# Kernel optimization log

Hardware: AMD Instinct MI355X
Metric: run time of the kernel (lower is better)

Reference implementation:

```python
import math
import jax, jax.numpy as jnp
import numpy as np

B, L, D_MODEL = 2, 2048, 1024
N_HEAD, HEAD_DIM = 16, 64
ATT_SCALE = 1.0  # divisor is sqrt(head_dim ** attention_scale)


def setup_inputs() -> dict:
    key = jax.random.key(0)
    ks = jax.random.split(key, 6)
    HD = N_HEAD * HEAD_DIM
    # Xavier-uniform style init for projection weights (stored as [in, out])
    def xavier(k, fan_in, fan_out):
        lim = math.sqrt(6.0 / (fan_in + fan_out))
        return jax.random.uniform(k, (fan_in, fan_out), jnp.float32, -lim, lim)
    return {
        "x":  jax.random.normal(ks[0], (B, L, D_MODEL), jnp.float32),
        "Wq": xavier(ks[1], D_MODEL, HD), "bq": jnp.zeros((HD,), jnp.float32),
        "Wk": xavier(ks[2], D_MODEL, HD), "bk": jnp.zeros((HD,), jnp.float32),
        "Wv": xavier(ks[3], D_MODEL, HD), "bv": jnp.zeros((HD,), jnp.float32),
        "Wo": xavier(ks[4], HD, D_MODEL),
        "bo": jax.random.uniform(ks[5], (D_MODEL,), jnp.float32, -1.0 / math.sqrt(HD), 1.0 / math.sqrt(HD)),
    }


def reference(x, Wq, bq, Wk, bk, Wv, bv, Wo, bo):
    b, l, _ = x.shape
    # QKV projections -> [B, L, H, Dh]
    q = (x @ Wq + bq).reshape(b, l, N_HEAD, HEAD_DIM)
    k = (x @ Wk + bk).reshape(b, l, N_HEAD, HEAD_DIM)
    v = (x @ Wv + bv).reshape(b, l, N_HEAD, HEAD_DIM)
    scale = 1.0 / math.sqrt(HEAD_DIM ** ATT_SCALE)
    # Unnormalized (no softmax) attention: (Q K^T / sqrt(Dh)) V
    scores = jnp.einsum("blhd,bmhd->bhlm", q, k) * scale  # [B,H,L,L]
    attn = jnp.einsum("bhlm,bmhd->blhd", scores, v)        # [B,L,H,Dh]
    out = attn.reshape(b, l, N_HEAD * HEAD_DIM) @ Wo + bo  # dispatcher
    return out
```

## Files before the change

### kernel.cpp

```cpp
#include <hip/hip_runtime.h>
#include <stdint.h>

#define B_ 2
#define L_ 2048
#define DM 1024
#define NH 16
#define DH 64
#define M_ (B_*L_)
#define NQKV 3072

typedef short short8 __attribute__((ext_vector_type(8)));
typedef float f32x4 __attribute__((ext_vector_type(4)));

__device__ __forceinline__ unsigned short f2b(float f) {
    union { float f; unsigned int u; } v; v.f = f;
    unsigned int u = v.u;
    return (unsigned short)((u + 0x7fffu + ((u >> 16) & 1u)) >> 16);
}

__device__ __forceinline__ void gld_lds16(const void* g, void* l) {
    __builtin_amdgcn_global_load_lds(
        (const __attribute__((address_space(1))) void*)g,
        (__attribute__((address_space(3))) void*)l, 16, 0, 0);
}

__global__ __launch_bounds__(256)
void setup_kernel(const float* __restrict__ x,
                  const float* __restrict__ Wq, const float* __restrict__ Wk,
                  const float* __restrict__ Wv, const float* __restrict__ Wo,
                  const float* __restrict__ bq, const float* __restrict__ bk,
                  const float* __restrict__ bv,
                  unsigned short* __restrict__ xb, unsigned short* __restrict__ WqkvT,
                  unsigned short* __restrict__ WoT, float* __restrict__ biasq,
                  float* __restrict__ KtV)
{
    __shared__ float tile[32][33];
    const int bid = blockIdx.x;
    const int t = threadIdx.x;

    if (bid < 2048) {
        int i = (bid * 256 + t) * 8;
        float4 a0 = *(const float4*)(x + i);
        float4 a1 = *(const float4*)(x + i + 4);
        uint4 p;
        p.x = (unsigned)f2b(a0.x) | ((unsigned)f2b(a0.y) << 16);
        p.y = (unsigned)f2b(a0.z) | ((unsigned)f2b(a0.w) << 16);
        p.z = (unsigned)f2b(a1.x) | ((unsigned)f2b(a1.y) << 16);
        p.w = (unsigned)f2b(a1.z) | ((unsigned)f2b(a1.w) << 16);
        *(uint4*)(xb + i) = p;
    } else if (bid < 2048 + 4096) {
        int wb = bid - 2048;
        int wi = wb >> 10;
        int tid = wb & 1023;
        const float* W = (wi == 0) ? Wq : (wi == 1) ? Wk : (wi == 2) ? Wv : Wo;
        float s = (wi == 1) ? 0.125f : 1.0f;
        int n0 = (tid & 31) * 32, k0 = (tid >> 5) * 32;
        int r = t >> 3, c4 = (t & 7) << 2;
        float4 v = *(const float4*)(W + (size_t)(k0 + r) * DM + n0 + c4);
        tile[r][c4+0] = v.x; tile[r][c4+1] = v.y; tile[r][c4+2] = v.z; tile[r][c4+3] = v.w;
        __syncthreads();
        uint2 o;
        o.x = (unsigned)f2b(tile[c4+0][r]*s) | ((unsigned)f2b(tile[c4+1][r]*s) << 16);
        o.y = (unsigned)f2b(tile[c4+2][r]*s) | ((unsigned)f2b(tile[c4+3][r]*s) << 16);
        int f = n0 + r;
        size_t drow;
        unsigned short* dst;
        if (wi == 0)      { dst = WqkvT; drow = f; }
        else if (wi == 1) { dst = WqkvT; drow = 1024 + (f >> 6) * 128 + (f & 63); }
        else if (wi == 2) { dst = WqkvT; drow = 1024 + (f >> 6) * 128 + 64 + (f & 63); }
        else              { dst = WoT;   drow = f; }
        *(uint2*)(dst + drow * DM + k0 + c4) = o;
    } else if (bid < 2048 + 4096 + 12) {
        int n = (bid - 6144) * 256 + t;
        float v;
        if (n < 1024) v = bq[n];
        else {
            int kv = (n - 1024) >> 7, r = (n - 1024) & 127;
            v = (r < 64) ? 0.125f * bk[kv * 64 + r] : bv[kv * 64 + (r - 64)];
        }
        biasq[n] = v;
    } else {
        int i = ((bid - 6156) * 256 + t) * 4;
        float4 z; z.x = z.y = z.z = z.w = 0.f;
        *(float4*)(KtV + i) = z;
    }
}

__global__ __launch_bounds__(256)
void qkv_fused_kernel(const unsigned short* __restrict__ A,
                      const unsigned short* __restrict__ Bt,
                      const float* __restrict__ biasq,
                      unsigned short* __restrict__ Qb,
                      float* __restrict__ KtV)
{
    __shared__ __align__(16) char smem[34816];
    unsigned short* As = (unsigned short*)smem;
    unsigned short* Bs = (unsigned short*)(smem + 8192);

    const int bid = blockIdx.x;
    const int xcd = bid & 7, local = bid >> 3;
    const int mt = xcd * 4 + (local & 3);
    const int nt = local >> 2;
    const int m0 = mt * 128, n0 = nt * 128;

    const int t = threadIdx.x;
    const int w = t >> 6, lane = t & 63;
    const int quad = lane >> 4, l16 = lane & 15;
    const int wm = w >> 1, wn = w & 1;

    f32x4 acc[4][4];
    #pragma unroll
    for (int i = 0; i < 4; i++)
        #pragma unroll
        for (int j = 0; j < 4; j++)
            #pragma unroll
            for (int r = 0; r < 4; r++) acc[i][j][r] = 0.f;

    const int srow = t >> 2;
    const int schunk = t & 3;

    for (int kk = 0; kk < DM; kk += 32) {
        #pragma unroll
        for (int p = 0; p < 2; p++) {
            int row = p * 64 + srow;
            int g = schunk ^ ((row >> 1) & 3);
            gld_lds16(A  + (size_t)(m0 + row) * DM + kk + g * 8,
                      (char*)As + p * 4096 + w * 1024);
            gld_lds16(Bt + (size_t)(n0 + row) * DM + kk + g * 8,
                      (char*)Bs + p * 4096 + w * 1024);
        }
        __syncthreads();

        short8 afr[4], bfr[4];
        #pragma unroll
        for (int i = 0; i < 4; i++) {
            int am = wm * 64 + i * 16 + l16;
            afr[i] = *(const short8*)((const char*)As + am * 64 + ((quad ^ ((am >> 1) & 3)) << 4));
            int bn = wn * 64 + i * 16 + l16;
            bfr[i] = *(const short8*)((const char*)Bs + bn * 64 + ((quad ^ ((bn >> 1) & 3)) << 4));
        }
        #pragma unroll
        for (int i = 0; i < 4; i++)
            #pragma unroll
            for (int j = 0; j < 4; j++)
                acc[i][j] = __builtin_amdgcn_mfma_f32_16x16x32_bf16(afr[i], bfr[j], acc[i][j], 0, 0, 0);
        __syncthreads();
    }

    #pragma unroll
    for (int j = 0; j < 4; j++) {
        float bv = biasq[n0 + wn * 64 + j * 16 + l16];
        #pragma unroll
        for (int i = 0; i < 4; i++)
            #pragma unroll
            for (int r = 0; r < 4; r++) acc[i][j][r] += bv;
    }

    if (nt < 8) {
        #pragma unroll
        for (int j = 0; j < 4; j++) {
            int col = n0 + wn * 64 + j * 16 + l16;
            #pragma unroll
            for (int i = 0; i < 4; i++) {
                #pragma unroll
                for (int r = 0; r < 4; r++) {
                    int row = m0 + wm * 64 + i * 16 + quad * 4 + r;
                    Qb[(size_t)row * DM + col] = f2b(acc[i][j][r]);
                }
            }
        }
        return;
    }

    const int h  = nt - 8;
    const int bh = (m0 >> 11) * NH + h;
    unsigned short (*Xt)[136] = (unsigned short (*)[136])smem;

    #pragma unroll
    for (int j = 0; j < 4; j++) {
        int c = wn * 64 + j * 16 + l16;
        #pragma unroll
        for (int i = 0; i < 4; i++) {
            int l0 = wm * 64 + i * 16 + quad * 4;
            uint2 o;
            o.x = (unsigned)f2b(acc[i][j][0]) | ((unsigned)f2b(acc[i][j][1]) << 16);
            o.y = (unsigned)f2b(acc[i][j][2]) | ((unsigned)f2b(acc[i][j][3]) << 16);
            *(uint2*)&Xt[c][l0] = o;
        }
    }
    __syncthreads();

    f32x4 kacc[4];
    #pragma unroll
    for (int j = 0; j < 4; j++)
        #pragma unroll
        for (int r = 0; r < 4; r++) kacc[j][r] = 0.f;

    #pragma unroll
    for (int ks = 0; ks < 4; ks++) {
        short8 af = *(const short8*)&Xt[w * 16 + l16][ks * 32 + quad * 8];
        #pragma unroll
        for (int j = 0; j < 4; j++) {
            short8 bfr = *(const short8*)&Xt[64 + j * 16 + l16][ks * 32 + quad * 8];
            kacc[j] = __builtin_amdgcn_mfma_f32_16x16x32_bf16(af, bfr, kacc[j], 0, 0, 0);
        }
    }

    float* dst = KtV + (size_t)bh * 64 * 64;
    #pragma unroll
    for (int j = 0; j < 4; j++) {
        int col = j * 16 + l16;
        #pragma unroll
        for (int r = 0; r < 4; r++) {
            int row = w * 16 + quad * 4 + r;
            atomicAdd(dst + row * 64 + col, kacc[j][r]);
        }
    }
}

__global__ __launch_bounds__(256)
void zmat_kernel(const unsigned short* __restrict__ WoT, const float* __restrict__ KtV,
                 unsigned short* __restrict__ ZT)
{
    __shared__ __align__(16) unsigned short Asl[64][72];
    __shared__ __align__(16) unsigned short Bsl[64][72];

    const int bh = blockIdx.x, nt0 = blockIdx.y;
    const int b = bh >> 4, h = bh & 15;
    const int t = threadIdx.x;
    const int wave = t >> 6, lane = t & 63;
    const int quad = lane >> 4, l16 = lane & 15;
    const int n0 = nt0 * 64;
    const int row = t >> 2, c0 = (t & 3) << 4;

    const unsigned short* ap = WoT + (size_t)(n0 + row) * DM + h * DH + c0;
    *(uint4*)&Asl[row][c0]     = *(const uint4*)ap;
    *(uint4*)&Asl[row][c0 + 8] = *(const uint4*)(ap + 8);

    const float* kp = KtV + ((size_t)bh * 64 + row) * 64 + c0;
    #pragma unroll
    for (int j = 0; j < 16; j++) Bsl[row][c0 + j] = f2b(kp[j]);
    __syncthreads();

    f32x4 acc[4];
    #pragma unroll
    for (int i = 0; i < 4; i++)
        #pragma unroll
        for (int r = 0; r < 4; r++) acc[i][r] = 0.f;

    #pragma unroll
    for (int ks = 0; ks < 2; ks++) {
        short8 af = *(const short8*)&Asl[wave * 16 + l16][ks * 32 + quad * 8];
        #pragma unroll
        for (int nt = 0; nt < 4; nt++) {
            short8 bfr = *(const short8*)&Bsl[nt * 16 + l16][ks * 32 + quad * 8];
            acc[nt] = __builtin_amdgcn_mfma_f32_16x16x32_bf16(af, bfr, acc[nt], 0, 0, 0);
        }
    }

    unsigned short* zb = ZT + (size_t)b * 1024 * 1024 + (size_t)h * DH;
    #pragma unroll
    for (int nt = 0; nt < 4; nt++) {
        int col = nt * 16 + l16;
        #pragma unroll
        for (int r = 0; r < 4; r++) {
            int zr = n0 + wave * 16 + quad * 4 + r;
            zb[(size_t)zr * 1024 + col] = f2b(acc[nt][r]);
        }
    }
}

__global__ __launch_bounds__(256)
void out_gemm_kernel(const unsigned short* __restrict__ A,
                     const unsigned short* __restrict__ Bt,
                     const float* __restrict__ bias,
                     float* __restrict__ C)
{
    __shared__ __align__(16) unsigned short As[128 * 64];
    __shared__ __align__(16) unsigned short Bs[64 * 64];

    const int bid = blockIdx.x;
    const int xcd = bid & 7, local = bid >> 3;
    const int mt = xcd * 4 + (local & 3);
    const int nt = local >> 2;
    const int m0 = mt * 128, n0 = nt * 64;

    const int t = threadIdx.x;
    const int w = t >> 6, lane = t & 63;
    const int quad = lane >> 4, l16 = lane & 15;

    const unsigned short* Btb = Bt + (size_t)(m0 >> 11) * 1024 * 1024;

    f32x4 acc[2][4];
    #pragma unroll
    for (int i = 0; i < 2; i++)
        #pragma unroll
        for (int j = 0; j < 4; j++)
            #pragma unroll
            for (int r = 0; r < 4; r++) acc[i][j][r] = 0.f;

    for (int kk = 0; kk < DM; kk += 64) {
        #pragma unroll
        for (int p = 0; p < 4; p++) {
            int c = p * 256 + t;
            int row = c >> 3, slot = c & 7;
            int g = slot ^ ((row >> 1) & 7);
            gld_lds16(A + (size_t)(m0 + row) * DM + kk + g * 8,
                      (char*)As + p * 4096 + w * 1024);
        }
        #pragma unroll
        for (int p = 0; p < 2; p++) {
            int c = p * 256 + t;
            int row = c >> 3, slot = c & 7;
            int g = slot ^ ((row >> 1) & 7);
            gld_lds16(Btb + (size_t)(n0 + row) * DM + kk + g * 8,
                      (char*)Bs + p * 4096 + w * 1024);
        }
        __syncthreads();

        #pragma unroll
        for (int ks = 0; ks < 2; ks++) {
            int kc = ks * 4 + quad;
            short8 afr[2], bfr[4];
            #pragma unroll
            for (int i = 0; i < 2; i++) {
                int am = w * 32 + i * 16 + l16;
                afr[i] = *(const short8*)((const char*)As + am * 128 + ((kc ^ ((am >> 1) & 7)) << 4));
            }
            #pragma unroll
            for (int j = 0; j < 4; j++) {
                int bn = j * 16 + l16;
                bfr[j] = *(const short8*)((const char*)Bs + bn * 128 + ((kc ^ ((bn >> 1) & 7)) << 4));
            }
            #pragma unroll
            for (int i = 0; i < 2; i++)
                #pragma unroll
                for (int j = 0; j < 4; j++)
                    acc[i][j] = __builtin_amdgcn_mfma_f32_16x16x32_bf16(afr[i], bfr[j], acc[i][j], 0, 0, 0);
        }
        __syncthreads();
    }

    #pragma unroll
    for (int j = 0; j < 4; j++) {
        int col = n0 + j * 16 + l16;
        float bv = bias[col];
        #pragma unroll
        for (int i = 0; i < 2; i++) {
            #pragma unroll
            for (int r = 0; r < 4; r++) {
                int row = m0 + w * 32 + i * 16 + quad * 4 + r;
                C[(size_t)row * DM + col] = acc[i][j][r] + bv;
            }
        }
    }
}


extern "C" void kernel_launch(void* const* d_in, const int* in_sizes, int n_in,
                              void* d_out, int out_size, void* d_ws, size_t ws_size,
                              hipStream_t stream)
{
    const float* x  = (const float*)d_in[0];
    const float* Wq = (const float*)d_in[1];
    const float* bq = (const float*)d_in[2];
    const float* Wk = (const float*)d_in[3];
    const float* bk = (const float*)d_in[4];
    const float* Wv = (const float*)d_in[5];
    const float* bv = (const float*)d_in[6];
    const float* Wo = (const float*)d_in[7];
    const float* bo = (const float*)d_in[8];

    char* ws = (char*)d_ws;
    unsigned short* xb    = (unsigned short*)(ws);
    unsigned short* WqkvT = (unsigned short*)(ws + (size_t)8  * 1024 * 1024);
    unsigned short* WoT   = (unsigned short*)(ws + (size_t)14 * 1024 * 1024);
    float*          biasq = (float*)         (ws + (size_t)16 * 1024 * 1024);
    unsigned short* Qb    = (unsigned short*)(ws + (size_t)17 * 1024 * 1024);
    unsigned short* ZT    = (unsigned short*)(ws + (size_t)25 * 1024 * 1024);
    float*          KtV   = (float*)         (ws + (size_t)29 * 1024 * 1024);

    setup_kernel<<<6284, 256, 0, stream>>>(x, Wq, Wk, Wv, Wo, bq, bk, bv,
                                           xb, WqkvT, WoT, biasq, KtV);

    qkv_fused_kernel<<<768, 256, 0, stream>>>(xb, WqkvT, biasq, Qb, KtV);

    zmat_kernel<<<dim3(B_ * NH, 16), 256, 0, stream>>>(WoT, KtV, ZT);

    out_gemm_kernel<<<512, 256, 0, stream>>>(Qb, ZT, bo, (float*)d_out);
}
```

Baseline: 143.3 us.

## Enlarge QKV GEMM tiles to 256x256 with double-buffered async LDS prefetch

The fused QKV GEMM now uses 256x256 output tiles with 512 threads, a 64-wide K step and two LDS buffers. Global-to-LDS loads for the next K step are issued while the current step's MFMAs run, with explicit vmcnt waits and barriers. The transposed K/V epilogue is reworked for two heads per tile and uses XOR-swizzled LDS. The aim is more data reuse per block and hidden load latency. In exchange only 192 blocks launch, which may underfill the GPU's CUs, and the 128 KB of LDS with the large accumulator array limits occupancy.

Measured after the change: 148.1 us. +3.4%, slower.

```diff
diff --git a/kernel.cpp b/kernel.cpp
--- a/kernel.cpp
+++ b/kernel.cpp
@@ -86,85 +86,112 @@
     }
 }
 
-__global__ __launch_bounds__(256)
+__global__ __launch_bounds__(512, 2)
 void qkv_fused_kernel(const unsigned short* __restrict__ A,
                       const unsigned short* __restrict__ Bt,
                       const float* __restrict__ biasq,
                       unsigned short* __restrict__ Qb,
                       float* __restrict__ KtV)
 {
-    __shared__ __align__(16) char smem[34816];
-    unsigned short* As = (unsigned short*)smem;
-    unsigned short* Bs = (unsigned short*)(smem + 8192);
+    __shared__ __align__(16) char smem[131072];
 
     const int bid = blockIdx.x;
-    const int xcd = bid & 7, local = bid >> 3;
-    const int mt = xcd * 4 + (local & 3);
-    const int nt = local >> 2;
-    const int m0 = mt * 128, n0 = nt * 128;
+    const int mt = bid & 15;
+    const int nt = bid >> 4;
+    const int m0 = mt * 256, n0 = nt * 256;
 
     const int t = threadIdx.x;
     const int w = t >> 6, lane = t & 63;
     const int quad = lane >> 4, l16 = lane & 15;
-    const int wm = w >> 1, wn = w & 1;
-
-    f32x4 acc[4][4];
-    #pragma unroll
-    for (int i = 0; i < 4; i++)
+    const int wr = w >> 2, wc = w & 3;
+
+    f32x4 acc[8][4];
+    #pragma unroll
+    for (int i = 0; i < 8; i++)
         #pragma unroll
         for (int j = 0; j < 4; j++)
             #pragma unroll
             for (int r = 0; r < 4; r++) acc[i][j][r] = 0.f;
 
-    const int srow = t >> 2;
-    const int schunk = t & 3;
-
-    for (int kk = 0; kk < DM; kk += 32) {
-        #pragma unroll
-        for (int p = 0; p < 2; p++) {
-            int row = p * 64 + srow;
-            int g = schunk ^ ((row >> 1) & 3);
-            gld_lds16(A  + (size_t)(m0 + row) * DM + kk + g * 8,
-                      (char*)As + p * 4096 + w * 1024);
+    auto STAGE = [&](int buf, int kk) {
+        #pragma unroll
+        for (int p = 0; p < 4; p++) {
+            int c = p * 512 + t;
+            int row = c >> 3, slot = c & 7;
+            int g = slot ^ ((row >> 1) & 7);
+            gld_lds16(A + (size_t)(m0 + row) * DM + kk + g * 8,
+                      smem + buf * 65536 + p * 8192 + w * 1024);
+        }
+        #pragma unroll
+        for (int p = 0; p < 4; p++) {
+            int c = p * 512 + t;
+            int row = c >> 3, slot = c & 7;
+            int g = slot ^ ((row >> 1) & 7);
             gld_lds16(Bt + (size_t)(n0 + row) * DM + kk + g * 8,
-                      (char*)Bs + p * 4096 + w * 1024);
-        }
-        __syncthreads();
-
-        short8 afr[4], bfr[4];
-        #pragma unroll
-        for (int i = 0; i < 4; i++) {
-            int am = wm * 64 + i * 16 + l16;
-            afr[i] = *(const short8*)((const char*)As + am * 64 + ((quad ^ ((am >> 1) & 3)) << 4));
-            int bn = wn * 64 + i * 16 + l16;
-            bfr[i] = *(const short8*)((const char*)Bs + bn * 64 + ((quad ^ ((bn >> 1) & 3)) << 4));
-        }
-        #pragma unroll
-        for (int i = 0; i < 4; i++)
-            #pragma unroll
-            for (int j = 0; j < 4; j++)
-                acc[i][j] = __builtin_amdgcn_mfma_f32_16x16x32_bf16(afr[i], bfr[j], acc[i][j], 0, 0, 0);
-        __syncthreads();
+                      smem + buf * 65536 + 32768 + p * 8192 + w * 1024);
+        }
+    };
+
+    STAGE(0, 0);
+    STAGE(1, 64);
+    asm volatile("s_waitcnt vmcnt(8)" ::: "memory");
+    __builtin_amdgcn_sched_barrier(0);
+    __builtin_amdgcn_s_barrier();
+
+    for (int T = 0; T < 16; T++) {
+        const char* Ab = smem + (T & 1) * 65536;
+        const char* Bb = Ab + 32768;
+        #pragma unroll
+        for (int kf = 0; kf < 2; kf++) {
+            int kc = kf * 4 + quad;
+            short8 af[8], bf[4];
+            #pragma unroll
+            for (int i = 0; i < 8; i++) {
+                int am = wr * 128 + i * 16 + l16;
+                af[i] = *(const short8*)(Ab + am * 128 + ((kc ^ ((am >> 1) & 7)) << 4));
+            }
+            #pragma unroll
+            for (int j = 0; j < 4; j++) {
+                int bn = wc * 64 + j * 16 + l16;
+                bf[j] = *(const short8*)(Bb + bn * 128 + ((kc ^ ((bn >> 1) & 7)) << 4));
+            }
+            #pragma unroll
+            for (int i = 0; i < 8; i++)
+                #pragma unroll
+                for (int j = 0; j < 4; j++)
+                    acc[i][j] = __builtin_amdgcn_mfma_f32_16x16x32_bf16(af[i], bf[j], acc[i][j], 0, 0, 0);
+        }
+        __builtin_amdgcn_sched_barrier(0);
+        __builtin_amdgcn_s_barrier();
+        if (T < 14) {
+            STAGE(T & 1, (T + 2) * 64);
+            __builtin_amdgcn_sched_barrier(0);
+            asm volatile("s_waitcnt vmcnt(8)" ::: "memory");
+        } else {
+            asm volatile("s_waitcnt vmcnt(0)" ::: "memory");
+        }
+        __builtin_amdgcn_sched_barrier(0);
+        __builtin_amdgcn_s_barrier();
     }
 
     #pragma unroll
     for (int j = 0; j < 4; j++) {
-        float bv = biasq[n0 + wn * 64 + j * 16 + l16];
-        #pragma unroll
-        for (int i = 0; i < 4; i++)
+        float bv = biasq[n0 + wc * 64 + j * 16 + l16];
+        #pragma unroll
+        for (int i = 0; i < 8; i++)
             #pragma unroll
             for (int r = 0; r < 4; r++) acc[i][j][r] += bv;
     }
 
-    if (nt < 8) {
+    if (nt < 4) {
         #pragma unroll
         for (int j = 0; j < 4; j++) {
-            int col = n0 + wn * 64 + j * 16 + l16;
-            #pragma unroll
-            for (int i = 0; i < 4; i++) {
+            int col = n0 + wc * 64 + j * 16 + l16;
+            #pragma unroll
+            for (int i = 0; i < 8; i++) {
                 #pragma unroll
                 for (int r = 0; r < 4; r++) {
-                    int row = m0 + wm * 64 + i * 16 + quad * 4 + r;
+                    int row = m0 + wr * 128 + i * 16 + quad * 4 + r;
                     Qb[(size_t)row * DM + col] = f2b(acc[i][j][r]);
                 }
             }
@@ -172,23 +199,26 @@
         return;
     }
 
-    const int h  = nt - 8;
-    const int bh = (m0 >> 11) * NH + h;
-    unsigned short (*Xt)[136] = (unsigned short (*)[136])smem;
-
     #pragma unroll
     for (int j = 0; j < 4; j++) {
-        int c = wn * 64 + j * 16 + l16;
-        #pragma unroll
-        for (int i = 0; i < 4; i++) {
-            int l0 = wm * 64 + i * 16 + quad * 4;
+        int c = wc * 64 + j * 16 + l16;
+        int cs = (c & 7) << 4;
+        #pragma unroll
+        for (int i = 0; i < 8; i++) {
+            int l0 = wr * 128 + i * 16 + quad * 4;
             uint2 o;
             o.x = (unsigned)f2b(acc[i][j][0]) | ((unsigned)f2b(acc[i][j][1]) << 16);
             o.y = (unsigned)f2b(acc[i][j][2]) | ((unsigned)f2b(acc[i][j][3]) << 16);
-            *(uint2*)&Xt[c][l0] = o;
-        }
-    }
-    __syncthreads();
+            *(uint2*)(smem + c * 512 + ((l0 * 2) ^ cs)) = o;
+        }
+    }
+    __builtin_amdgcn_sched_barrier(0);
+    __builtin_amdgcn_s_barrier();
+
+    const int hh = w >> 2;
+    const int s  = w & 3;
+    const int bb = mt >> 3;
+    const int h  = (nt - 4) * 2 + hh;
 
     f32x4 kacc[4];
     #pragma unroll
@@ -197,22 +227,24 @@
         for (int r = 0; r < 4; r++) kacc[j][r] = 0.f;
 
     #pragma unroll
-    for (int ks = 0; ks < 4; ks++) {
-        short8 af = *(const short8*)&Xt[w * 16 + l16][ks * 32 + quad * 8];
+    for (int ks = 0; ks < 8; ks++) {
+        int ca = hh * 128 + s * 16 + l16;
+        short8 afk = *(const short8*)(smem + ca * 512 + ((ks * 64 + quad * 16) ^ ((ca & 7) << 4)));
         #pragma unroll
         for (int j = 0; j < 4; j++) {
-            short8 bfr = *(const short8*)&Xt[64 + j * 16 + l16][ks * 32 + quad * 8];
-            kacc[j] = __builtin_amdgcn_mfma_f32_16x16x32_bf16(af, bfr, kacc[j], 0, 0, 0);
-        }
-    }
-
-    float* dst = KtV + (size_t)bh * 64 * 64;
+            int cb = hh * 128 + 64 + j * 16 + l16;
+            short8 bfk = *(const short8*)(smem + cb * 512 + ((ks * 64 + quad * 16) ^ ((cb & 7) << 4)));
+            kacc[j] = __builtin_amdgcn_mfma_f32_16x16x32_bf16(afk, bfk, kacc[j], 0, 0, 0);
+        }
+    }
+
+    float* dst = KtV + (size_t)(bb * NH + h) * 64 * 64;
     #pragma unroll
     for (int j = 0; j < 4; j++) {
         int col = j * 16 + l16;
         #pragma unroll
         for (int r = 0; r < 4; r++) {
-            int row = w * 16 + quad * 4 + r;
+            int row = s * 16 + quad * 4 + r;
             atomicAdd(dst + row * 64 + col, kacc[j][r]);
         }
     }
@@ -383,7 +415,7 @@
     setup_kernel<<<6284, 256, 0, stream>>>(x, Wq, Wk, Wv, Wo, bq, bk, bv,
                                            xb, WqkvT, WoT, biasq, KtV);
 
-    qkv_fused_kernel<<<768, 256, 0, stream>>>(xb, WqkvT, biasq, Qb, KtV);
+    qkv_fused_kernel<<<192, 512, 0, stream>>>(xb, WqkvT, biasq, Qb, KtV);
 
     zmat_kernel<<<dim3(B_ * NH, 16), 256, 0, stream>>>(WoT, KtV, ZT);
 
```
